# Optimization experiments

Measured on AMD Instinct MI355X. Metric: run time of the kernel, lower is better.

The kernel has to match this reference:

```python
import jax, jax.numpy as jnp
import numpy as np

B, D, N = 2, 256, 8192   # batch, in_channels, sequence length
CI = 128                 # inter_channels
BN_EPS = 1e-5


def conv1x1(w, b, x):
    # w: (Cout, Cin), b: (Cout,), x: (B, Cin, N) -> (B, Cout, N)
    return jnp.einsum('oc,bcn->bon', w, x) + b[None, :, None]


def maxpool2(x):
    # MaxPool1d(kernel_size=2): (B, C, N) -> (B, C, N//2)
    b, c, n = x.shape
    return x.reshape(b, c, n // 2, 2).max(axis=-1)


def setup_inputs() -> dict:
    key = jax.random.key(0)
    ks = jax.random.split(key, 11)
    s_in = 1.0 / np.sqrt(D)
    s_ci = 1.0 / np.sqrt(CI)
    return {
        'f': jax.random.normal(ks[0], (B, D, N), dtype=jnp.float32),
        'g_w': jax.random.uniform(ks[1], (CI, D), jnp.float32, -s_in, s_in),
        'g_b': jax.random.uniform(ks[2], (CI,), jnp.float32, -s_in, s_in),
        'theta_w': jax.random.uniform(ks[3], (CI, D), jnp.float32, -s_in, s_in),
        'theta_b': jax.random.uniform(ks[4], (CI,), jnp.float32, -s_in, s_in),
        'phi_w': jax.random.uniform(ks[5], (CI, D), jnp.float32, -s_in, s_in),
        'phi_b': jax.random.uniform(ks[6], (CI,), jnp.float32, -s_in, s_in),
        'W_w': jax.random.uniform(ks[7], (D, CI), jnp.float32, -s_ci, s_ci),
        'W_b': jax.random.uniform(ks[8], (D,), jnp.float32, -s_ci, s_ci),
        'bn_gamma': jax.random.normal(ks[9], (D,), dtype=jnp.float32) * 0.1,
        'bn_beta': jax.random.normal(ks[10], (D,), dtype=jnp.float32) * 0.1,
    }


def reference(f, g_w, g_b, theta_w, theta_b, phi_w, phi_b, W_w, W_b, bn_gamma, bn_beta):
    # projections (1x1 convs); g and phi are sub-sampled by maxpool(2)
    g_f = maxpool2(conv1x1(g_w, g_b, f))          # (B, CI, N/2)
    theta_f = conv1x1(theta_w, theta_b, f)        # (B, CI, N)
    phi_f = maxpool2(conv1x1(phi_w, phi_b, f))    # (B, CI, N/2)

    # affinity: theta^T @ phi, softmax over keys (no scale, as in source)
    A = jnp.einsum('bcn,bcm->bnm', theta_f, phi_f)     # (B, N, N/2)
    A = jax.nn.softmax(A, axis=-1)
    y = jnp.einsum('bnm,bcm->bcn', A, g_f)             # (B, CI, N)

    # W: 1x1 conv + BatchNorm1d (training-mode batch stats), residual
    Wy = conv1x1(W_w, W_b, y)                          # (B, D, N)
    mean = Wy.mean(axis=(0, 2), keepdims=True)
    var = Wy.var(axis=(0, 2), keepdims=True)           # biased, like torch BN
    Wy = (Wy - mean) * jax.lax.rsqrt(var + BN_EPS)
    Wy = Wy * bn_gamma[None, :, None] + bn_beta[None, :, None]
    return Wy + f
```

## Files before the change

### kernel.cpp

```cpp
#include <hip/hip_runtime.h>
#include <hip/hip_bf16.h>
#include <math.h>

#define B_ 2
#define D_ 256
#define N_ 8192
#define CI_ 128
#define M_ 4096
#define BN_EPS_ 1e-5f
#define LOG2E_ 1.4426950408889634f

#define GLOBAL_AS __attribute__((address_space(1)))
#define LDS_AS __attribute__((address_space(3)))

#define OFF_WALL 0
#define OFF_THT  65536
#define OFF_PHT  (OFF_THT + 1048576)
#define OFF_GT   (OFF_PHT + 524288)
#define OFF_YP   (OFF_GT  + 524288)

typedef __attribute__((ext_vector_type(8))) short bfrag;
typedef __attribute__((ext_vector_type(4))) float f4v;
typedef __attribute__((ext_vector_type(16))) float f16v;
typedef __attribute__((ext_vector_type(4))) short s4v;
typedef __attribute__((ext_vector_type(4))) unsigned u4v;

__device__ inline unsigned short bf16rne(float x) {
    unsigned u = __float_as_uint(x);
    u += 0x7fff + ((u >> 16) & 1);
    return (unsigned short)(u >> 16);
}

__device__ inline float exp2fast(float x) {
    float r;
    asm("v_exp_f32 %0, %1" : "=v"(r) : "v"(x));
    return r;
}

__global__ __launch_bounds__(256) void wconv_kernel(
    const float* __restrict__ gw, const float* __restrict__ tw, const float* __restrict__ pw,
    const float* __restrict__ Ww, short* __restrict__ wall)
{
    int idx = blockIdx.x * 256 + threadIdx.x;
    int which = idx >> 15;
    int rem = idx & 32767;
    const float* src = (which == 0) ? gw : (which == 1) ? tw : (which == 2) ? pw : Ww;
    float v = src[rem];
    if (which == 1) v *= LOG2E_;
    wall[idx] = (short)bf16rne(v);
}

__global__ __launch_bounds__(256, 2) void proj_kernel(
    const float* __restrict__ f, const short* __restrict__ wall,
    const float* __restrict__ tb, const float* __restrict__ gb, const float* __restrict__ pb,
    short* __restrict__ th_t, short* __restrict__ g_t, short* __restrict__ ph_t)
{
    __shared__ short sF[32 * 72];

    const int tid = threadIdx.x;
    const int wave = tid >> 6, lane = tid & 63;
    const int lq = lane & 15, quad = lane >> 4;
    const int b = blockIdx.y;
    const int n0 = blockIdx.x * 32;

    const float* fb = f + (size_t)b * D_ * N_;

    f4v acc[6][2];
#pragma unroll
    for (int ct = 0; ct < 6; ct++)
#pragma unroll
        for (int nf = 0; nf < 2; nf++) acc[ct][nf] = (f4v){0.f, 0.f, 0.f, 0.f};

    const int sn = tid & 31;
    const int sgrp = tid >> 5;

    for (int kc = 0; kc < D_; kc += 64) {
        __syncthreads();
#pragma unroll
        for (int jj = 0; jj < 4; jj++) {
            int dd = kc + sgrp * 8 + 2 * jj;
            float v0 = fb[(size_t)dd * N_ + n0 + sn];
            float v1 = fb[(size_t)(dd + 1) * N_ + n0 + sn];
            unsigned pk = (unsigned)bf16rne(v0) | ((unsigned)bf16rne(v1) << 16);
            *(unsigned*)&sF[sn * 72 + sgrp * 8 + 2 * jj] = pk;
        }
        __syncthreads();

        bfrag afr[6][2], bfr[2][2];
#pragma unroll
        for (int ks = 0; ks < 2; ks++) {
#pragma unroll
            for (int nf = 0; nf < 2; nf++)
                bfr[nf][ks] = *(const bfrag*)&sF[(nf * 16 + lq) * 72 + ks * 32 + quad * 8];
#pragma unroll
            for (int ct = 0; ct < 6; ct++)
                afr[ct][ks] = *(const bfrag*)&wall[(wave * 96 + ct * 16 + lq) * 256 + kc + ks * 32 + quad * 8];
        }
#pragma unroll
        for (int ks = 0; ks < 2; ks++)
#pragma unroll
            for (int ct = 0; ct < 6; ct++) {
                acc[ct][0] = __builtin_amdgcn_mfma_f32_16x16x32_bf16(afr[ct][ks], bfr[0][ks], acc[ct][0], 0, 0, 0);
                acc[ct][1] = __builtin_amdgcn_mfma_f32_16x16x32_bf16(afr[ct][ks], bfr[1][ks], acc[ct][1], 0, 0, 0);
            }
    }

#pragma unroll
    for (int ct = 0; ct < 6; ct++) {
        const int cf = wave * 6 + ct;
#pragma unroll
        for (int nf = 0; nf < 2; nf++) {
            f4v v = acc[ct][nf];
            const int n = n0 + nf * 16 + lq;
            if (cf < 8) {
                const int cb = cf * 16 + quad * 4;
                float pl[4];
#pragma unroll
                for (int r = 0; r < 4; r++) {
                    float o = __shfl_xor(v[r], 1);
                    pl[r] = fmaxf(v[r], o) + gb[cb + r];
                }
                if (!(lq & 1)) {
                    const int m = n >> 1;
#pragma unroll
                    for (int r = 0; r < 4; r++)
                        g_t[((size_t)b * CI_ + cb + r) * M_ + m] = (short)bf16rne(pl[r]);
                }
            } else if (cf < 16) {
                const int cb = (cf - 8) * 16 + quad * 4;
                s4v o;
#pragma unroll
                for (int r = 0; r < 4; r++) o[r] = (short)bf16rne(v[r] + tb[cb + r] * LOG2E_);
                *(s4v*)&th_t[((size_t)b * N_ + n) * CI_ + cb] = o;
            } else {
                const int cb = (cf - 16) * 16 + quad * 4;
                float pl[4];
#pragma unroll
                for (int r = 0; r < 4; r++) {
                    float o = __shfl_xor(v[r], 1);
                    pl[r] = fmaxf(v[r], o) + pb[cb + r];
                }
                if (!(lq & 1)) {
                    const int m = n >> 1;
                    s4v o;
#pragma unroll
                    for (int r = 0; r < 4; r++) o[r] = (short)bf16rne(pl[r]);
                    *(s4v*)&ph_t[((size_t)b * M_ + m) * CI_ + cb] = o;
                }
            }
        }
    }
}

template<int NS>
__global__ __launch_bounds__(256, 3) void attn_kernel(
    const short* __restrict__ th_p, const short* __restrict__ ph_p,
    const short* __restrict__ g_p, short* __restrict__ yp, float* __restrict__ ml)
{
    __shared__ short sPh[2][32 * 128];
    __shared__ short sG [2][128 * 40];

    const int tid = threadIdx.x;
    const int wave = tid >> 6, lane = tid & 63;
    const int l = lane & 31, h = lane >> 5;

    const int bid = blockIdx.x;
    const int pair = bid % (2 * NS);
    const int b = pair & 1;
    const int split = pair >> 1;
    const int q0 = (bid / (2 * NS)) * 128;
    const int qg = q0 + wave * 32 + l;

    int k0, SK;
    if (NS == 6) {
        if (split < 2) { SK = 704; k0 = split * 704; }
        else           { SK = 672; k0 = 1408 + (split - 2) * 672; }
    } else {
        SK = M_ / NS; k0 = split * SK;
    }

    const short* thr = th_p + ((size_t)b * N_ + qg) * CI_;
    bfrag tf[8];
#pragma unroll
    for (int s = 0; s < 8; s++)
        tf[s] = *(const bfrag*)&thr[s * 16 + h * 8];

    f16v yacc[4];
#pragma unroll
    for (int ct = 0; ct < 4; ct++)
#pragma unroll
        for (int r = 0; r < 16; r++) yacc[ct][r] = 0.f;
    float mI = -INFINITY, lI = 0.f;

    const short* phg = ph_p + (size_t)b * M_ * CI_;
    const short* gg  = g_p + (size_t)b * CI_ * M_;

    const int xm = l & 15;

    const int prow = (lane >> 4);
    const int pslot = lane & 15;

    const int i0 = (wave < 2) ? wave * 3 : 6 + (wave - 2) * 2;
    const int nIss = (wave < 2) ? 3 : 2;
    int gsrc[3];
#pragma unroll
    for (int p = 0; p < 3; p++) {
        const int t = (i0 + p) * 64 + lane;
        gsrc[p] = (t / 5) * M_ + (t % 5) * 8;
    }

#define STAGE_DMA(BUF, KC)                                                                  \
    do {                                                                                    \
        _Pragma("unroll")                                                                   \
        for (int p = 0; p < 2; p++) {                                                       \
            const int rp = wave * 8 + p * 4 + prow;                      \
            const int cg = pslot ^ (rp & 15);                        \
            __builtin_amdgcn_global_load_lds(                                               \
                (const GLOBAL_AS void*)(phg + (size_t)((KC) + rp) * 128 + cg * 8),          \
                (LDS_AS void*)(&sPh[BUF][(wave * 8 + p * 4) * 128]), 16, 0, 0);             \
        }                                                                                   \
        _Pragma("unroll")                                                                   \
        for (int p = 0; p < 3; p++) {                                                       \
            if (p < nIss)                                                                   \
                __builtin_amdgcn_global_load_lds(                                           \
                    (const GLOBAL_AS void*)(gg + gsrc[p] + (KC)),                           \
                    (LDS_AS void*)(&sG[BUF][(i0 + p) * 512]), 16, 0, 0);                    \
        }                                                                                   \
    } while (0)

    STAGE_DMA(0, k0);

    int cur = 0;
    for (int kc = k0; kc < k0 + SK; kc += 32) {
        __syncthreads();
        const bool nxt = (kc + 32 < k0 + SK);
        if (nxt) {
            STAGE_DMA(cur ^ 1, kc + 32);
            __builtin_amdgcn_sched_barrier(0);
        }

        f16v sv;
#pragma unroll
        for (int r = 0; r < 16; r++) sv[r] = 0.f;
        __builtin_amdgcn_s_setprio(1);
#pragma unroll
        for (int s = 0; s < 8; s++) {
            bfrag pa = *(const bfrag*)&sPh[cur][l * 128 + (((s << 1) | h) ^ xm) * 8];
            sv = __builtin_amdgcn_mfma_f32_32x32x16_bf16(pa, tf[s], sv, 0, 0, 0);
        }
        __builtin_amdgcn_s_setprio(0);

        float mx;
        {
            float t[8];
#pragma unroll
            for (int r = 0; r < 8; r++) t[r] = fmaxf(sv[r], sv[r + 8]);
#pragma unroll
            for (int st = 4; st > 0; st >>= 1)
#pragma unroll
                for (int r = 0; r < st; r++) t[r] = fmaxf(t[r], t[r + st]);
            mx = fmaxf(t[0], __shfl_xor(t[0], 32));
        }

        if (__any(mx > mI + 8.f)) {
            float mnew = fmaxf(mI, mx);
            float al = exp2fast(mI - mnew);
            lI *= al;
#pragma unroll
            for (int ct = 0; ct < 4; ct++)
#pragma unroll
                for (int r = 0; r < 16; r++) yacc[ct][r] *= al;
            mI = mnew;
        }

        float ps = 0.f;
        bfrag pf[2];
#pragma unroll
        for (int s = 0; s < 2; s++) {
            const int rb = s * 8;
            float p[8];
#pragma unroll
            for (int j = 0; j < 8; j++) p[j] = exp2fast(sv[rb + j] - mI);
            ps += ((p[0] + p[1]) + (p[2] + p[3])) + ((p[4] + p[5]) + (p[6] + p[7]));
            unsigned w0, w1, w2, w3;
            asm("v_cvt_pk_bf16_f32 %0, %1, %2" : "=v"(w0) : "v"(p[0]), "v"(p[1]));
            asm("v_cvt_pk_bf16_f32 %0, %1, %2" : "=v"(w1) : "v"(p[2]), "v"(p[3]));
            asm("v_cvt_pk_bf16_f32 %0, %1, %2" : "=v"(w2) : "v"(p[4]), "v"(p[5]));
            asm("v_cvt_pk_bf16_f32 %0, %1, %2" : "=v"(w3) : "v"(p[6]), "v"(p[7]));
            unsigned O0 = h ? w2 : w0;
            unsigned O1 = h ? w3 : w1;
            unsigned Xs0 = h ? w0 : w2;
            unsigned Xs1 = h ? w1 : w3;
            unsigned X0 = (unsigned)__shfl_xor((int)Xs0, 32);
            unsigned X1 = (unsigned)__shfl_xor((int)Xs1, 32);
            u4v t;
            t.x = h ? X0 : O0;
            t.y = h ? X1 : O1;
            t.z = h ? O0 : X0;
            t.w = h ? O1 : X1;
            pf[s] = __builtin_bit_cast(bfrag, t);
        }
        ps += __shfl_xor(ps, 32);
        lI += ps;

        __builtin_amdgcn_s_setprio(1);
#pragma unroll
        for (int ct = 0; ct < 4; ct++)
#pragma unroll
            for (int s = 0; s < 2; s++) {
                bfrag ga = *(const bfrag*)&sG[cur][(ct * 32 + l) * 40 + s * 16 + h * 8];
                yacc[ct] = __builtin_amdgcn_mfma_f32_32x32x16_bf16(ga, pf[s], yacc[ct], 0, 0, 0);
            }
        __builtin_amdgcn_s_setprio(0);

        cur ^= 1;
    }
#undef STAGE_DMA

    short* yb = yp + (((size_t)split * B_ + b) * N_) * CI_;
#pragma unroll
    for (int ct = 0; ct < 4; ct++)
#pragma unroll
        for (int rq = 0; rq < 4; rq++) {
            const int c0 = ct * 32 + 8 * rq + 4 * h;
            s4v o;
#pragma unroll
            for (int j = 0; j < 4; j++) o[j] = (short)bf16rne(yacc[ct][rq * 4 + j]);
            *(s4v*)&yb[(size_t)qg * CI_ + c0] = o;
        }
    if (h == 0) {
        float* mlb = ml + ((split * B_ + b) * 2) * N_;
        mlb[qg] = mI;
        mlb[N_ + qg] = lI;
    }
}

template<int NS>
__global__ __launch_bounds__(256) void wy_merge_kernel(
    const short* __restrict__ yp, const float* __restrict__ ml,
    const short* __restrict__ wall2, const float* __restrict__ Wb,
    float* __restrict__ out)
{
    const int tid = threadIdx.x;
    const int wave = tid >> 6, lane = tid & 63;
    const int l = lane & 31, h = lane >> 5;
    const int b = blockIdx.y;
    const int n = blockIdx.x * 32 + l;

    float m[NS], lv[NS];
#pragma unroll
    for (int sp = 0; sp < NS; sp++) {
        const float* mlb = ml + ((sp * B_ + b) * 2) * N_;
        m[sp] = mlb[n];
        lv[sp] = mlb[N_ + n];
    }
    float mmax = m[0];
#pragma unroll
    for (int sp = 1; sp < NS; sp++) mmax = fmaxf(mmax, m[sp]);
    float e[NS], den = 0.f;
#pragma unroll
    for (int sp = 0; sp < NS; sp++) { e[sp] = exp2fast(m[sp] - mmax); den += lv[sp] * e[sp]; }
    float inv = 1.0f / den;
#pragma unroll
    for (int sp = 0; sp < NS; sp++) e[sp] *= inv;

    bfrag by[8];
#pragma unroll
    for (int s = 0; s < 8; s++) {
        float a[8];
#pragma unroll
        for (int j = 0; j < 8; j++) a[j] = 0.f;
#pragma unroll
        for (int sp = 0; sp < NS; sp++) {
            bfrag yv = *(const bfrag*)&yp[(((size_t)sp * B_ + b) * N_ + n) * CI_ + s * 16 + h * 8];
            u4v u = __builtin_bit_cast(u4v, yv);
#pragma unroll
            for (int p = 0; p < 4; p++) {
                a[2 * p]     = fmaf(e[sp], __uint_as_float(u[p] << 16), a[2 * p]);
                a[2 * p + 1] = fmaf(e[sp], __uint_as_float(u[p] & 0xffff0000u), a[2 * p + 1]);
            }
        }
        u4v pk;
#pragma unroll
        for (int p = 0; p < 4; p++) {
            unsigned r;
            asm("v_cvt_pk_bf16_f32 %0, %1, %2" : "=v"(r) : "v"(a[2 * p]), "v"(a[2 * p + 1]));
            pk[p] = r;
        }
        by[s] = __builtin_bit_cast(bfrag, pk);
    }

    f16v acc[2];
#pragma unroll
    for (int rt = 0; rt < 2; rt++)
#pragma unroll
        for (int r = 0; r < 16; r++) acc[rt][r] = 0.f;

#pragma unroll
    for (int s = 0; s < 8; s++)
#pragma unroll
        for (int rt = 0; rt < 2; rt++) {
            bfrag aw = *(const bfrag*)&wall2[((wave * 2 + rt) * 32 + l) * 128 + s * 16 + h * 8];
            acc[rt] = __builtin_amdgcn_mfma_f32_32x32x16_bf16(aw, by[s], acc[rt], 0, 0, 0);
        }

#pragma unroll
    for (int rt = 0; rt < 2; rt++)
#pragma unroll
        for (int r = 0; r < 16; r++) {
            const int d = (wave * 2 + rt) * 32 + (r & 3) + 8 * (r >> 2) + 4 * h;
            out[((size_t)b * D_ + d) * N_ + n] = acc[rt][r] + Wb[d];
        }
}

__global__ __launch_bounds__(256) void stats_kernel(
    const float* __restrict__ wy, float* __restrict__ mean, float* __restrict__ rstd)
{
    __shared__ float ssum[256], ssq[256];
    int d = blockIdx.x;
    int tid = threadIdx.x;
    float s = 0.f, sq = 0.f;
    for (int b = 0; b < B_; b++) {
        const float4* p = (const float4*)(wy + (size_t)b * D_ * N_ + (size_t)d * N_);
        for (int i = tid; i < N_ / 4; i += 256) {
            float4 v = p[i];
            s += v.x + v.y + v.z + v.w;
            sq = fmaf(v.x, v.x, sq);
            sq = fmaf(v.y, v.y, sq);
            sq = fmaf(v.z, v.z, sq);
            sq = fmaf(v.w, v.w, sq);
        }
    }
    ssum[tid] = s; ssq[tid] = sq;
    __syncthreads();
    for (int st = 128; st > 0; st >>= 1) {
        if (tid < st) { ssum[tid] += ssum[tid + st]; ssq[tid] += ssq[tid + st]; }
        __syncthreads();
    }
    if (tid == 0) {
        float inv = 1.0f / (float)(B_ * N_);
        float mn = ssum[0] * inv;
        float var = ssq[0] * inv - mn * mn;
        mean[d] = mn;
        rstd[d] = rsqrtf(var + BN_EPS_);
    }
}

__global__ __launch_bounds__(256) void bn_res_kernel(
    float* __restrict__ out, const float* __restrict__ f,
    const float* __restrict__ mean, const float* __restrict__ rstd,
    const float* __restrict__ gamma, const float* __restrict__ beta)
{
    int i = blockIdx.x * 256 + threadIdx.x;
    size_t e = (size_t)i * 4;
    int d = (int)((e >> 13) & 255);
    float4 wy = ((const float4*)out)[i];
    float4 ff = ((const float4*)f)[i];
    float sc = rstd[d] * gamma[d];
    float mn = mean[d];
    float bt = beta[d];
    float4 r;
    r.x = (wy.x - mn) * sc + bt + ff.x;
    r.y = (wy.y - mn) * sc + bt + ff.y;
    r.z = (wy.z - mn) * sc + bt + ff.z;
    r.w = (wy.w - mn) * sc + bt + ff.w;
    ((float4*)out)[i] = r;
}

extern "C" void kernel_launch(void* const* d_in, const int* in_sizes, int n_in,
                              void* d_out, int out_size, void* d_ws, size_t ws_size,
                              hipStream_t stream)
{
    const float* f   = (const float*)d_in[0];
    const float* g_w = (const float*)d_in[1];
    const float* g_b = (const float*)d_in[2];
    const float* t_w = (const float*)d_in[3];
    const float* t_b = (const float*)d_in[4];
    const float* p_w = (const float*)d_in[5];
    const float* p_b = (const float*)d_in[6];
    const float* W_w = (const float*)d_in[7];
    const float* W_b = (const float*)d_in[8];
    const float* gam = (const float*)d_in[9];
    const float* bet = (const float*)d_in[10];
    float* out = (float*)d_out;
    float* ws = (float*)d_ws;

    const size_t need6 = ((size_t)OFF_YP + 6u * 1048576u + 6u * 32768u + 512u) * 4u;
    const int ns = (ws_size >= need6) ? 6 : 4;

    short* wall  = (short*)(ws + OFF_WALL);
    short* wall2 = wall + 3 * 32768;
    short* th_t = (short*)(ws + OFF_THT);
    short* ph_t = (short*)(ws + OFF_PHT);
    short* g_t  = (short*)(ws + OFF_GT);
    short* ypart = (short*)(ws + OFF_YP);
    float* mlp = ws + OFF_YP + (size_t)ns * 1048576u;
    float* mnp = mlp + (size_t)ns * 32768u;
    float* rsp = mnp + 256;

    wconv_kernel<<<512, 256, 0, stream>>>(g_w, t_w, p_w, W_w, wall);
    proj_kernel<<<dim3(N_ / 32, B_), 256, 0, stream>>>(f, wall, t_b, g_b, p_b,
                                                       th_t, g_t, ph_t);
    if (ns == 6) {
        attn_kernel<6><<<768, 256, 0, stream>>>(th_t, ph_t, g_t, ypart, mlp);
        wy_merge_kernel<6><<<dim3(N_ / 32, B_), 256, 0, stream>>>(ypart, mlp, wall2, W_b, out);
    } else {
        attn_kernel<4><<<512, 256, 0, stream>>>(th_t, ph_t, g_t, ypart, mlp);
        wy_merge_kernel<4><<<dim3(N_ / 32, B_), 256, 0, stream>>>(ypart, mlp, wall2, W_b, out);
    }
    stats_kernel<<<D_, 256, 0, stream>>>(out, mnp, rsp);
    bn_res_kernel<<<(B_ * D_ * N_ / 4) / 256, 256, 0, stream>>>(out, f, mnp, rsp, gam, bet);
}
```

Measured before the change: 185.6 us.

## Process two query tiles per wave in attention to reuse staged K/V tiles

Each wave now handles 64 queries (two 32-row tiles) instead of 32, so every phi and g fragment loaded from LDS feeds two MFMAs, doubling compute per staged byte. The key split count rises from 6 to 8 with an even split and the grid is recomputed, which keeps the block count at 512. Register pressure doubles for accumulators, so launch bounds drop from 3 to 2 blocks per CU, lowering occupancy and latency hiding. The merge kernel must combine more partial results, and the workspace requirement grows.

```diff
diff --git a/kernel.cpp b/kernel.cpp
--- a/kernel.cpp
+++ b/kernel.cpp
@@ -153,10 +153,11 @@
 }
 
 template<int NS>
-__global__ __launch_bounds__(256, 3) void attn_kernel(
+__global__ __launch_bounds__(256, 2) void attn_kernel(
     const short* __restrict__ th_p, const short* __restrict__ ph_p,
     const short* __restrict__ g_p, short* __restrict__ yp, float* __restrict__ ml)
 {
+    constexpr int SK = M_ / NS;
     __shared__ short sPh[2][32 * 128];
     __shared__ short sG [2][128 * 40];
 
@@ -168,29 +169,26 @@
     const int pair = bid % (2 * NS);
     const int b = pair & 1;
     const int split = pair >> 1;
-    const int q0 = (bid / (2 * NS)) * 128;
-    const int qg = q0 + wave * 32 + l;
-
-    int k0, SK;
-    if (NS == 6) {
-        if (split < 2) { SK = 704; k0 = split * 704; }
-        else           { SK = 672; k0 = 1408 + (split - 2) * 672; }
-    } else {
-        SK = M_ / NS; k0 = split * SK;
-    }
-
-    const short* thr = th_p + ((size_t)b * N_ + qg) * CI_;
-    bfrag tf[8];
-#pragma unroll
-    for (int s = 0; s < 8; s++)
-        tf[s] = *(const bfrag*)&thr[s * 16 + h * 8];
-
-    f16v yacc[4];
+    const int q0 = (bid / (2 * NS)) * 256;
+    const int qga = q0 + wave * 64 + l;
+    const int k0 = split * SK;
+
+    bfrag tf0[8], tf1[8];
+    {
+        const short* t0 = th_p + ((size_t)b * N_ + qga) * CI_;
+#pragma unroll
+        for (int s = 0; s < 8; s++) tf0[s] = *(const bfrag*)&t0[s * 16 + h * 8];
+        const short* t1 = t0 + 32 * CI_;
+#pragma unroll
+        for (int s = 0; s < 8; s++) tf1[s] = *(const bfrag*)&t1[s * 16 + h * 8];
+    }
+
+    f16v yacc0[4], yacc1[4];
 #pragma unroll
     for (int ct = 0; ct < 4; ct++)
 #pragma unroll
-        for (int r = 0; r < 16; r++) yacc[ct][r] = 0.f;
-    float mI = -INFINITY, lI = 0.f;
+        for (int r = 0; r < 16; r++) { yacc0[ct][r] = 0.f; yacc1[ct][r] = 0.f; }
+    float m0 = -INFINITY, l0 = 0.f, m1 = -INFINITY, l1 = 0.f;
 
     const short* phg = ph_p + (size_t)b * M_ * CI_;
     const short* gg  = g_p + (size_t)b * CI_ * M_;
@@ -230,6 +228,67 @@
 
     STAGE_DMA(0, k0);
 
+#define SOFTMAX_PF(SV, MI, LI, YA, PFA, PFB)                                                \
+    do {                                                                                    \
+        float t[8];                                                                         \
+        _Pragma("unroll")                                                                   \
+        for (int r = 0; r < 8; r++) t[r] = fmaxf(SV[r], SV[r + 8]);                         \
+        _Pragma("unroll")                                                                   \
+        for (int st = 4; st > 0; st >>= 1)                                                  \
+            _Pragma("unroll")                                                               \
+            for (int r = 0; r < st; r++) t[r] = fmaxf(t[r], t[r + st]);                     \
+        float mx = fmaxf(t[0], __shfl_xor(t[0], 32));                                       \
+        if (__any(mx > MI + 8.f)) {                                                         \
+            float mnew = fmaxf(MI, mx);                                                     \
+            float al = exp2fast(MI - mnew);                                                 \
+            LI *= al;                                                                       \
+            _Pragma("unroll")                                                               \
+            for (int ct = 0; ct < 4; ct++)                                                  \
+                _Pragma("unroll")                                                           \
+                for (int r = 0; r < 16; r++) YA[ct][r] *= al;                               \
+            MI = mnew;                                                                      \
+        }                                                                                   \
+        float ps = 0.f;                                                                     \
+        {                                                                                   \
+            float p[8];                                                                     \
+            _Pragma("unroll")                                                               \
+            for (int j = 0; j < 8; j++) p[j] = exp2fast(SV[j] - MI);                        \
+            ps += ((p[0] + p[1]) + (p[2] + p[3])) + ((p[4] + p[5]) + (p[6] + p[7]));        \
+            unsigned w0, w1, w2, w3;                                                        \
+            asm("v_cvt_pk_bf16_f32 %0, %1, %2" : "=v"(w0) : "v"(p[0]), "v"(p[1]));          \
+            asm("v_cvt_pk_bf16_f32 %0, %1, %2" : "=v"(w1) : "v"(p[2]), "v"(p[3]));          \
+            asm("v_cvt_pk_bf16_f32 %0, %1, %2" : "=v"(w2) : "v"(p[4]), "v"(p[5]));          \
+            asm("v_cvt_pk_bf16_f32 %0, %1, %2" : "=v"(w3) : "v"(p[6]), "v"(p[7]));          \
+            unsigned O0 = h ? w2 : w0;                                                      \
+            unsigned O1 = h ? w3 : w1;                                                      \
+            unsigned X0 = (unsigned)__shfl_xor((int)(h ? w0 : w2), 32);                     \
+            unsigned X1 = (unsigned)__shfl_xor((int)(h ? w1 : w3), 32);                     \
+            u4v u; u.x = h ? X0 : O0; u.y = h ? X1 : O1;                                    \
+            u.z = h ? O0 : X0; u.w = h ? O1 : X1;                                           \
+            PFA = __builtin_bit_cast(bfrag, u);                                             \
+        }                                                                                   \
+        {                                                                                   \
+            float p[8];                                                                     \
+            _Pragma("unroll")                                                               \
+            for (int j = 0; j < 8; j++) p[j] = exp2fast(SV[8 + j] - MI);                    \
+            ps += ((p[0] + p[1]) + (p[2] + p[3])) + ((p[4] + p[5]) + (p[6] + p[7]));        \
+            unsigned w0, w1, w2, w3;                                                        \
+            asm("v_cvt_pk_bf16_f32 %0, %1, %2" : "=v"(w0) : "v"(p[0]), "v"(p[1]));          \
+            asm("v_cvt_pk_bf16_f32 %0, %1, %2" : "=v"(w1) : "v"(p[2]), "v"(p[3]));          \
+            asm("v_cvt_pk_bf16_f32 %0, %1, %2" : "=v"(w2) : "v"(p[4]), "v"(p[5]));          \
+            asm("v_cvt_pk_bf16_f32 %0, %1, %2" : "=v"(w3) : "v"(p[6]), "v"(p[7]));          \
+            unsigned O0 = h ? w2 : w0;                                                      \
+            unsigned O1 = h ? w3 : w1;                                                      \
+            unsigned X0 = (unsigned)__shfl_xor((int)(h ? w0 : w2), 32);                     \
+            unsigned X1 = (unsigned)__shfl_xor((int)(h ? w1 : w3), 32);                     \
+            u4v u; u.x = h ? X0 : O0; u.y = h ? X1 : O1;                                    \
+            u.z = h ? O0 : X0; u.w = h ? O1 : X1;                                           \
+            PFB = __builtin_bit_cast(bfrag, u);                                             \
+        }                                                                                   \
+        ps += __shfl_xor(ps, 32);                                                           \
+        LI += ps;                                                                           \
+    } while (0)
+
     int cur = 0;
     for (int kc = k0; kc < k0 + SK; kc += 32) {
         __syncthreads();
@@ -239,83 +298,38 @@
             __builtin_amdgcn_sched_barrier(0);
         }
 
-        f16v sv;
-#pragma unroll
-        for (int r = 0; r < 16; r++) sv[r] = 0.f;
+        f16v sv0, sv1;
+#pragma unroll
+        for (int r = 0; r < 16; r++) { sv0[r] = 0.f; sv1[r] = 0.f; }
         __builtin_amdgcn_s_setprio(1);
 #pragma unroll
         for (int s = 0; s < 8; s++) {
             bfrag pa = *(const bfrag*)&sPh[cur][l * 128 + (((s << 1) | h) ^ xm) * 8];
-            sv = __builtin_amdgcn_mfma_f32_32x32x16_bf16(pa, tf[s], sv, 0, 0, 0);
+            sv0 = __builtin_amdgcn_mfma_f32_32x32x16_bf16(pa, tf0[s], sv0, 0, 0, 0);
+            sv1 = __builtin_amdgcn_mfma_f32_32x32x16_bf16(pa, tf1[s], sv1, 0, 0, 0);
         }
         __builtin_amdgcn_s_setprio(0);
 
-        float mx;
-        {
-            float t[8];
-#pragma unroll
-            for (int r = 0; r < 8; r++) t[r] = fmaxf(sv[r], sv[r + 8]);
-#pragma unroll
-            for (int st = 4; st > 0; st >>= 1)
-#pragma unroll
-                for (int r = 0; r < st; r++) t[r] = fmaxf(t[r], t[r + st]);
-            mx = fmaxf(t[0], __shfl_xor(t[0], 32));
-        }
-
-        if (__any(mx > mI + 8.f)) {
-            float mnew = fmaxf(mI, mx);
-            float al = exp2fast(mI - mnew);
-            lI *= al;
-#pragma unroll
-            for (int ct = 0; ct < 4; ct++)
-#pragma unroll
-                for (int r = 0; r < 16; r++) yacc[ct][r] *= al;
-            mI = mnew;
-        }
-
-        float ps = 0.f;
-        bfrag pf[2];
-#pragma unroll
-        for (int s = 0; s < 2; s++) {
-            const int rb = s * 8;
-            float p[8];
-#pragma unroll
-            for (int j = 0; j < 8; j++) p[j] = exp2fast(sv[rb + j] - mI);
-            ps += ((p[0] + p[1]) + (p[2] + p[3])) + ((p[4] + p[5]) + (p[6] + p[7]));
-            unsigned w0, w1, w2, w3;
-            asm("v_cvt_pk_bf16_f32 %0, %1, %2" : "=v"(w0) : "v"(p[0]), "v"(p[1]));
-            asm("v_cvt_pk_bf16_f32 %0, %1, %2" : "=v"(w1) : "v"(p[2]), "v"(p[3]));
-            asm("v_cvt_pk_bf16_f32 %0, %1, %2" : "=v"(w2) : "v"(p[4]), "v"(p[5]));
-            asm("v_cvt_pk_bf16_f32 %0, %1, %2" : "=v"(w3) : "v"(p[6]), "v"(p[7]));
-            unsigned O0 = h ? w2 : w0;
-            unsigned O1 = h ? w3 : w1;
-            unsigned Xs0 = h ? w0 : w2;
-            unsigned Xs1 = h ? w1 : w3;
-            unsigned X0 = (unsigned)__shfl_xor((int)Xs0, 32);
-            unsigned X1 = (unsigned)__shfl_xor((int)Xs1, 32);
-            u4v t;
-            t.x = h ? X0 : O0;
-            t.y = h ? X1 : O1;
-            t.z = h ? O0 : X0;
-            t.w = h ? O1 : X1;
-            pf[s] = __builtin_bit_cast(bfrag, t);
-        }
-        ps += __shfl_xor(ps, 32);
-        lI += ps;
+        bfrag pf0a, pf0b, pf1a, pf1b;
+        SOFTMAX_PF(sv0, m0, l0, yacc0, pf0a, pf0b);
+        SOFTMAX_PF(sv1, m1, l1, yacc1, pf1a, pf1b);
 
         __builtin_amdgcn_s_setprio(1);
 #pragma unroll
-        for (int ct = 0; ct < 4; ct++)
-#pragma unroll
-            for (int s = 0; s < 2; s++) {
-                bfrag ga = *(const bfrag*)&sG[cur][(ct * 32 + l) * 40 + s * 16 + h * 8];
-                yacc[ct] = __builtin_amdgcn_mfma_f32_32x32x16_bf16(ga, pf[s], yacc[ct], 0, 0, 0);
-            }
+        for (int ct = 0; ct < 4; ct++) {
+            bfrag ga0 = *(const bfrag*)&sG[cur][(ct * 32 + l) * 40 + h * 8];
+            yacc0[ct] = __builtin_amdgcn_mfma_f32_32x32x16_bf16(ga0, pf0a, yacc0[ct], 0, 0, 0);
+            yacc1[ct] = __builtin_amdgcn_mfma_f32_32x32x16_bf16(ga0, pf1a, yacc1[ct], 0, 0, 0);
+            bfrag ga1 = *(const bfrag*)&sG[cur][(ct * 32 + l) * 40 + 16 + h * 8];
+            yacc0[ct] = __builtin_amdgcn_mfma_f32_32x32x16_bf16(ga1, pf0b, yacc0[ct], 0, 0, 0);
+            yacc1[ct] = __builtin_amdgcn_mfma_f32_32x32x16_bf16(ga1, pf1b, yacc1[ct], 0, 0, 0);
+        }
         __builtin_amdgcn_s_setprio(0);
 
         cur ^= 1;
     }
 #undef STAGE_DMA
+#undef SOFTMAX_PF
 
     short* yb = yp + (((size_t)split * B_ + b) * N_) * CI_;
 #pragma unroll
@@ -323,15 +337,21 @@
 #pragma unroll
         for (int rq = 0; rq < 4; rq++) {
             const int c0 = ct * 32 + 8 * rq + 4 * h;
-            s4v o;
-#pragma unroll
-            for (int j = 0; j < 4; j++) o[j] = (short)bf16rne(yacc[ct][rq * 4 + j]);
-            *(s4v*)&yb[(size_t)qg * CI_ + c0] = o;
+            s4v o0, o1;
+#pragma unroll
+            for (int j = 0; j < 4; j++) {
+                o0[j] = (short)bf16rne(yacc0[ct][rq * 4 + j]);
+                o1[j] = (short)bf16rne(yacc1[ct][rq * 4 + j]);
+            }
+            *(s4v*)&yb[(size_t)qga * CI_ + c0] = o0;
+            *(s4v*)&yb[(size_t)(qga + 32) * CI_ + c0] = o1;
         }
     if (h == 0) {
         float* mlb = ml + ((split * B_ + b) * 2) * N_;
-        mlb[qg] = mI;
-        mlb[N_ + qg] = lI;
+        mlb[qga] = m0;
+        mlb[N_ + qga] = l0;
+        mlb[qga + 32] = m1;
+        mlb[N_ + qga + 32] = l1;
     }
 }
 
@@ -485,8 +505,8 @@
     float* out = (float*)d_out;
     float* ws = (float*)d_ws;
 
-    const size_t need6 = ((size_t)OFF_YP + 6u * 1048576u + 6u * 32768u + 512u) * 4u;
-    const int ns = (ws_size >= need6) ? 6 : 4;
+    const size_t need8 = ((size_t)OFF_YP + 8u * 1048576u + 8u * 32768u + 512u) * 4u;
+    const int ns = (ws_size >= need8) ? 8 : 4;
 
     short* wall  = (short*)(ws + OFF_WALL);
     short* wall2 = wall + 3 * 32768;
@@ -501,11 +521,11 @@
     wconv_kernel<<<512, 256, 0, stream>>>(g_w, t_w, p_w, W_w, wall);
     proj_kernel<<<dim3(N_ / 32, B_), 256, 0, stream>>>(f, wall, t_b, g_b, p_b,
                                                        th_t, g_t, ph_t);
-    if (ns == 6) {
-        attn_kernel<6><<<768, 256, 0, stream>>>(th_t, ph_t, g_t, ypart, mlp);
-        wy_merge_kernel<6><<<dim3(N_ / 32, B_), 256, 0, stream>>>(ypart, mlp, wall2, W_b, out);
+    if (ns == 8) {
+        attn_kernel<8><<<(N_ / 256) * B_ * 8, 256, 0, stream>>>(th_t, ph_t, g_t, ypart, mlp);
+        wy_merge_kernel<8><<<dim3(N_ / 32, B_), 256, 0, stream>>>(ypart, mlp, wall2, W_b, out);
     } else {
-        attn_kernel<4><<<512, 256, 0, stream>>>(th_t, ph_t, g_t, ypart, mlp);
+        attn_kernel<4><<<(N_ / 256) * B_ * 4, 256, 0, stream>>>(th_t, ph_t, g_t, ypart, mlp);
         wy_merge_kernel<4><<<dim3(N_ / 32, B_), 256, 0, stream>>>(ypart, mlp, wall2, W_b, out);
     }
     stats_kernel<<<D_, 256, 0, stream>>>(out, mnp, rsp);
```

New measurement: 210.6 us. 13.5% more time.
